# Performance work log

Hardware: AMD Instinct MI355X
Metric: run time of the kernel (lower is better)

The kernel has to match this reference:

```python
import jax, jax.numpy as jnp
import numpy as np

N = 10000
E = 640000


def setup_inputs() -> dict:
    key = jax.random.key(0)
    k = jax.random.split(key, 6)
    x = jax.random.normal(k[0], (N, 128), dtype=jnp.float32)
    edge_index = jax.random.randint(k[1], (2, E), 0, N, dtype=jnp.int64)
    # Linear weights stored as [in, out] (torch stores [out, in]; math is x @ W.T + b)
    w1 = jax.random.normal(k[2], (128, 128), dtype=jnp.float32) * 0.05
    b1 = jax.random.normal(k[3], (128,), dtype=jnp.float32) * 0.05
    w2 = jax.random.normal(k[4], (128, 128), dtype=jnp.float32) * 0.05
    b2 = jax.random.normal(k[5], (128,), dtype=jnp.float32) * 0.05
    return {"x": x, "edge_index": edge_index, "w1": w1, "b1": b1, "w2": w2, "b2": b2}


def gin_conv(x, src, dst, w, b, eps=0.0):
    # aggregate: out[i] = sum over edges (src->dst=i) of x[src]
    agg = jax.ops.segment_sum(x[src], dst, num_segments=N)  # [N, d]
    h = (1.0 + eps) * x + agg
    return h @ w + b


def reference(x, edge_index, w1, b1, w2, b2):
    src, dst = edge_index[0], edge_index[1]
    h = gin_conv(x, src, dst, w1, b1)
    h = jax.nn.relu(h)
    h = gin_conv(h, src, dst, w2, b2)
    return jax.nn.log_softmax(h, axis=1)
```

## Files before the change

kernel.cpp:

```cpp
#include <hip/hip_runtime.h>
#include <cstdint>

#define NNODES 10000
#define FDIM 128
#define MAXDEG 192
#define SLOTS 48

typedef _Float16 h2v  __attribute__((ext_vector_type(2)));
typedef _Float16 f16x8 __attribute__((ext_vector_type(8)));
typedef float    f32x4 __attribute__((ext_vector_type(4)));

__device__ __align__(16)  int      g_cnt[NNODES * 4];
__device__                int      g_bucket[NNODES * MAXDEG];
__device__ __align__(256) unsigned g_xh [(NNODES + 1) * FDIM / 2];
__device__ __align__(256) unsigned g_h1h[(NNODES + 1) * FDIM / 2];
__device__ __align__(16)  unsigned g_wf[2 * 8192];

__device__ inline h2v as_h2(unsigned u) { return __builtin_bit_cast(h2v, u); }
__device__ inline unsigned as_u(h2v v) { return __builtin_bit_cast(unsigned, v); }
__device__ inline unsigned pack_f16x2(float a, float b) {
  h2v v; v[0] = (_Float16)a; v[1] = (_Float16)b;
  return as_u(v);
}
__device__ inline void vadd4(uint4& a, const uint4& b) {
  a.x = as_u(as_h2(a.x) + as_h2(b.x));
  a.y = as_u(as_h2(a.y) + as_h2(b.y));
  a.z = as_u(as_h2(a.z) + as_h2(b.z));
  a.w = as_u(as_h2(a.w) + as_h2(b.w));
}

__global__ __launch_bounds__(256) void prep_kernel(
    const float* __restrict__ x, const int* __restrict__ ei,
    const float* __restrict__ w1, const float* __restrict__ w2,
    int E_, int EBLK, int CBLK) {
  const int bid = blockIdx.x;
  if (bid < EBLK) {
    int e = bid * 256 + threadIdx.x;
    if (e < E_) {
      int d = ei[E_ + e];
      int s = ei[e];
      int st = e & 3;
      int p = atomicAdd(&g_cnt[d * 4 + st], 1);
      if (p < SLOTS) g_bucket[d * MAXDEG + st * SLOTS + p] = s;
    }
  } else if (bid < EBLK + CBLK) {
    int i = (bid - EBLK) * 256 + threadIdx.x;
    if (i < NNODES * FDIM / 2) {
      float2 v = *(const float2*)(x + 2 * (size_t)i);
      g_xh[i] = pack_f16x2(v.x, v.y);
    }
  } else {
    int idx = (bid - EBLK - CBLK) * 256 + threadIdx.x;
    const float* w = (idx >= 2048) ? w2 : w1;
    int s = idx & 2047;
    int sl = s & 63, nk = s >> 6;
    int n = nk >> 2, kc = nk & 3;
    int kbase = kc * 32 + (sl >> 4) * 8;
    int f = n * 16 + (sl & 15);
    unsigned d0 = pack_f16x2(w[(size_t)(kbase + 0) * FDIM + f],
                             w[(size_t)(kbase + 1) * FDIM + f]);
    unsigned d1 = pack_f16x2(w[(size_t)(kbase + 2) * FDIM + f],
                             w[(size_t)(kbase + 3) * FDIM + f]);
    unsigned d2 = pack_f16x2(w[(size_t)(kbase + 4) * FDIM + f],
                             w[(size_t)(kbase + 5) * FDIM + f]);
    unsigned d3 = pack_f16x2(w[(size_t)(kbase + 6) * FDIM + f],
                             w[(size_t)(kbase + 7) * FDIM + f]);
    *(uint4*)(g_wf + (idx >> 11) * 8192 + 4 * s) = make_uint4(d0, d1, d2, d3);
  }
}

template <int MODE>
__global__ __launch_bounds__(512) void gin_layer_kernel(
    const float* __restrict__ b,
    float* __restrict__ out_g) {
  const unsigned* __restrict__ xh = (MODE == 0) ? g_xh : g_h1h;

  __shared__ __align__(16) unsigned wl[8192];
  __shared__ __align__(16) unsigned al[16 * 68];

  const int tid = threadIdx.x;
  const int wave = tid >> 6, lane = tid & 63;
  const int quad = lane >> 4, m16 = lane & 15;
  const int node0 = blockIdx.x * 16;

  {
    const uint4* wf4 = (const uint4*)(g_wf + (MODE ? 8192 : 0));
    uint4* wl4 = (uint4*)wl;
#pragma unroll
    for (int it = 0; it < 4; ++it) wl4[tid + it * 512] = wf4[tid + it * 512];
  }

  const int myn0 = node0 + wave * 2;
  uint4 self4[2];
  int o1[2], o2[2], o3[2], dgg[2];
#pragma unroll
  for (int i = 0; i < 2; ++i) {
    self4[i] = *(const uint4*)(xh + (size_t)(myn0 + i) * 64 + (m16 << 2));
    int4 c = *(const int4*)(g_cnt + (myn0 + i) * 4);
    int a = (c.x > SLOTS) ? SLOTS : c.x;
    int bq = (c.y > SLOTS) ? SLOTS : c.y;
    int cq = (c.z > SLOTS) ? SLOTS : c.z;
    int dq = (c.w > SLOTS) ? SLOTS : c.w;
    o1[i] = a; o2[i] = a + bq; o3[i] = a + bq + cq; dgg[i] = a + bq + cq + dq;
  }

  for (int i = 0; i < 2; ++i) {
    h2v a0 = as_h2(0u), a1 = as_h2(0u), a2 = as_h2(0u), a3 = as_h2(0u);
    const int deg = dgg[i];
    const int* nb = g_bucket + (size_t)(myn0 + i) * MAXDEG;
    for (int p = 0; p < deg; p += 64) {
      int n = deg - p; if (n > 64) n = 64;
      int myedge = NNODES;
      if (lane < n) {
        int g = p + lane;
        int base = 0;
        if (g >= o1[i]) base = o1[i];
        if (g >= o2[i]) base = o2[i];
        if (g >= o3[i]) base = o3[i];
        int st = (g >= o1[i]) + (g >= o2[i]) + (g >= o3[i]);
        myedge = nb[st * SLOTS + (g - base)];
      }
      const int nst = (n + 3) >> 2;
      int s = 0;
      for (; s + 8 <= nst; s += 8) {
        uint4 t[8];
#pragma unroll
        for (int k = 0; k < 8; ++k) {
          int e = __builtin_amdgcn_ds_bpermute((((s + k) << 2) | quad) << 2, myedge);
          t[k] = *(const uint4*)(xh + (unsigned)((e << 6) | (m16 << 2)));
        }
#pragma unroll
        for (int st2 = 1; st2 < 8; st2 <<= 1)
#pragma unroll
          for (int k = 0; k < 8; k += 2 * st2) vadd4(t[k], t[k + st2]);
        a0 += as_h2(t[0].x); a1 += as_h2(t[0].y);
        a2 += as_h2(t[0].z); a3 += as_h2(t[0].w);
      }
      if (s + 4 <= nst) {
        uint4 t[4];
#pragma unroll
        for (int k = 0; k < 4; ++k) {
          int e = __builtin_amdgcn_ds_bpermute((((s + k) << 2) | quad) << 2, myedge);
          t[k] = *(const uint4*)(xh + (unsigned)((e << 6) | (m16 << 2)));
        }
        vadd4(t[0], t[1]); vadd4(t[2], t[3]); vadd4(t[0], t[2]);
        a0 += as_h2(t[0].x); a1 += as_h2(t[0].y);
        a2 += as_h2(t[0].z); a3 += as_h2(t[0].w);
        s += 4;
      }
      for (; s < nst; ++s) {
        int e = __builtin_amdgcn_ds_bpermute(((s << 2) | quad) << 2, myedge);
        uint4 t = *(const uint4*)(xh + (unsigned)((e << 6) | (m16 << 2)));
        a0 += as_h2(t.x); a1 += as_h2(t.y); a2 += as_h2(t.z); a3 += as_h2(t.w);
      }
    }
    int r;
    r = __shfl_xor((int)as_u(a0), 16, 64); a0 += as_h2((unsigned)r);
    r = __shfl_xor((int)as_u(a0), 32, 64); a0 += as_h2((unsigned)r);
    r = __shfl_xor((int)as_u(a1), 16, 64); a1 += as_h2((unsigned)r);
    r = __shfl_xor((int)as_u(a1), 32, 64); a1 += as_h2((unsigned)r);
    r = __shfl_xor((int)as_u(a2), 16, 64); a2 += as_h2((unsigned)r);
    r = __shfl_xor((int)as_u(a2), 32, 64); a2 += as_h2((unsigned)r);
    r = __shfl_xor((int)as_u(a3), 16, 64); a3 += as_h2((unsigned)r);
    r = __shfl_xor((int)as_u(a3), 32, 64); a3 += as_h2((unsigned)r);
    a0 += as_h2(self4[i].x); a1 += as_h2(self4[i].y);
    a2 += as_h2(self4[i].z); a3 += as_h2(self4[i].w);
    if (quad == 0)
      *(uint4*)(al + (wave * 2 + i) * 68 + (m16 << 2)) =
          make_uint4(as_u(a0), as_u(a1), as_u(a2), as_u(a3));
  }
  __syncthreads();

  uint4 af[4];
#pragma unroll
  for (int kc = 0; kc < 4; ++kc)
    af[kc] = *(const uint4*)(al + m16 * 68 + kc * 16 + quad * 4);

  const int n = wave;
  const float bb = b[n * 16 + m16];
  f32x4 acc = {0.f, 0.f, 0.f, 0.f};
#pragma unroll
  for (int kc = 0; kc < 4; ++kc) {
    uint4 bf = *(const uint4*)(wl + ((n * 4 + kc) * 64 + lane) * 4);
    acc = __builtin_amdgcn_mfma_f32_16x16x32_f16(
            __builtin_bit_cast(f16x8, af[kc]),
            __builtin_bit_cast(f16x8, bf), acc, 0, 0, 0);
  }
  __syncthreads();

  if (MODE == 0) {
    _Float16* ch = (_Float16*)wl;
    const int f = n * 16 + m16;
#pragma unroll
    for (int reg = 0; reg < 4; ++reg)
      ch[(quad * 4 + reg) * 136 + f] = (_Float16)fmaxf(acc[reg] + bb, 0.f);
    __syncthreads();
    const int row = tid >> 5, c2 = (tid & 31) * 2;
    uint2 v = *(const uint2*)(wl + row * 68 + c2);
    *(uint2*)(&g_h1h[(size_t)(node0 + row) * 64 + c2]) = v;
  } else {
    float* cf = (float*)wl;
    const int f = n * 16 + m16;
#pragma unroll
    for (int reg = 0; reg < 4; ++reg)
      cf[(quad * 4 + reg) * 132 + f] = acc[reg] + bb;
    __syncthreads();
    const int row = tid >> 5, li = tid & 31;
    const float* base = cf + row * 132 + li * 4;
    float4 a4 = *(const float4*)(base);
    float mx = fmaxf(fmaxf(a4.x, a4.y), fmaxf(a4.z, a4.w));
#pragma unroll
    for (int off = 16; off >= 1; off >>= 1)
      mx = fmaxf(mx, __shfl_xor(mx, off, 64));
    float s = (__expf(a4.x - mx) + __expf(a4.y - mx))
            + (__expf(a4.z - mx) + __expf(a4.w - mx));
#pragma unroll
    for (int off = 16; off >= 1; off >>= 1)
      s += __shfl_xor(s, off, 64);
    const float ls = mx + __logf(s);
    float* orow = out_g + (size_t)(node0 + row) * FDIM + li * 4;
    *(float4*)(orow) = make_float4(a4.x - ls, a4.y - ls, a4.z - ls, a4.w - ls);
    if (tid < 64) g_cnt[node0 * 4 + tid] = 0;
  }
}

extern "C" void kernel_launch(void* const* d_in, const int* in_sizes, int n_in,
                              void* d_out, int out_size, void* d_ws, size_t ws_size,
                              hipStream_t stream) {
  const float* x  = (const float*)d_in[0];
  const int*   ei = (const int*)d_in[1];
  const float* w1 = (const float*)d_in[2];
  const float* b1 = (const float*)d_in[3];
  const float* w2 = (const float*)d_in[4];
  const float* b2 = (const float*)d_in[5];
  float* out = (float*)d_out;

  const int E_ = in_sizes[1] / 2;
  const int EBLK = (E_ + 255) / 256;
  const int CBLK = (NNODES * FDIM / 2 + 255) / 256;
  const int WBLK = 16;

  prep_kernel<<<EBLK + CBLK + WBLK, 256, 0, stream>>>(x, ei, w1, w2, E_, EBLK, CBLK);

  gin_layer_kernel<0><<<625, 512, 0, stream>>>(b1, nullptr);
  gin_layer_kernel<1><<<625, 512, 0, stream>>>(b2, out);
}
```

Before: 126.0 us.

## Fuse prep and both GIN layers into one cooperative persistent kernel

Replaces the three separate launches (prep, layer 0, layer 1) with a single cooperative kernel that uses grid-wide syncs between phases and grid-stride loops over node groups. Weight fragments are now held in registers per wave instead of being staged through shared memory each block, and the x-to-fp16 conversion is vectorised to float4. This removes launch gaps and per-block weight copies, but adds grid barrier cost and caps parallelism at the co-resident block count.

```diff
diff --git a/kernel.cpp b/kernel.cpp
--- a/kernel.cpp
+++ b/kernel.cpp
@@ -1,5 +1,8 @@
 #include <hip/hip_runtime.h>
+#include <hip/hip_cooperative_groups.h>
 #include <cstdint>
+
+namespace cg = cooperative_groups;
 
 #define NNODES 10000
 #define FDIM 128
@@ -29,28 +32,185 @@
   a.w = as_u(as_h2(a.w) + as_h2(b.w));
 }
 
-__global__ __launch_bounds__(256) void prep_kernel(
+template <int MODE>
+__device__ __forceinline__ void layer_phase(
+    const float* __restrict__ bvec, float* __restrict__ out_g,
+    unsigned* __restrict__ al,
+    unsigned* __restrict__ cfu) {
+  const unsigned* __restrict__ xh = (MODE == 0) ? g_xh : g_h1h;
+
+  const int tid = threadIdx.x;
+  const int wave = tid >> 6, lane = tid & 63;
+  const int quad = lane >> 4, m16 = lane & 15;
+
+  uint4 bf[4];
+  {
+    const unsigned* wfp = g_wf + (MODE ? 8192 : 0);
+#pragma unroll
+    for (int kc = 0; kc < 4; ++kc)
+      bf[kc] = *(const uint4*)(wfp + ((wave * 4 + kc) * 64 + lane) * 4);
+  }
+  const float bb = bvec[wave * 16 + m16];
+
+  for (int grp = blockIdx.x; grp < 625; grp += gridDim.x) {
+    const int node0 = grp * 16;
+    const int myn0 = node0 + wave * 2;
+
+    uint4 self4[2];
+    int o1[2], o2[2], o3[2], dgg[2];
+#pragma unroll
+    for (int i = 0; i < 2; ++i) {
+      self4[i] = *(const uint4*)(xh + (size_t)(myn0 + i) * 64 + (m16 << 2));
+      int4 c = *(const int4*)(g_cnt + (myn0 + i) * 4);
+      int a = (c.x > SLOTS) ? SLOTS : c.x;
+      int bq = (c.y > SLOTS) ? SLOTS : c.y;
+      int cq = (c.z > SLOTS) ? SLOTS : c.z;
+      int dq = (c.w > SLOTS) ? SLOTS : c.w;
+      o1[i] = a; o2[i] = a + bq; o3[i] = a + bq + cq; dgg[i] = a + bq + cq + dq;
+    }
+
+    for (int i = 0; i < 2; ++i) {
+      h2v a0 = as_h2(0u), a1 = as_h2(0u), a2 = as_h2(0u), a3 = as_h2(0u);
+      const int deg = dgg[i];
+      const int* nb = g_bucket + (size_t)(myn0 + i) * MAXDEG;
+      for (int p = 0; p < deg; p += 64) {
+        int n = deg - p; if (n > 64) n = 64;
+        int myedge = NNODES;
+        if (lane < n) {
+          int g = p + lane;
+          int base = 0;
+          if (g >= o1[i]) base = o1[i];
+          if (g >= o2[i]) base = o2[i];
+          if (g >= o3[i]) base = o3[i];
+          int st = (g >= o1[i]) + (g >= o2[i]) + (g >= o3[i]);
+          myedge = nb[st * SLOTS + (g - base)];
+        }
+        const int nst = (n + 3) >> 2;
+        int s = 0;
+        for (; s + 8 <= nst; s += 8) {
+          uint4 t[8];
+#pragma unroll
+          for (int k = 0; k < 8; ++k) {
+            int e = __builtin_amdgcn_ds_bpermute((((s + k) << 2) | quad) << 2, myedge);
+            t[k] = *(const uint4*)(xh + (unsigned)((e << 6) | (m16 << 2)));
+          }
+#pragma unroll
+          for (int st2 = 1; st2 < 8; st2 <<= 1)
+#pragma unroll
+            for (int k = 0; k < 8; k += 2 * st2) vadd4(t[k], t[k + st2]);
+          a0 += as_h2(t[0].x); a1 += as_h2(t[0].y);
+          a2 += as_h2(t[0].z); a3 += as_h2(t[0].w);
+        }
+        if (s + 4 <= nst) {
+          uint4 t[4];
+#pragma unroll
+          for (int k = 0; k < 4; ++k) {
+            int e = __builtin_amdgcn_ds_bpermute((((s + k) << 2) | quad) << 2, myedge);
+            t[k] = *(const uint4*)(xh + (unsigned)((e << 6) | (m16 << 2)));
+          }
+          vadd4(t[0], t[1]); vadd4(t[2], t[3]); vadd4(t[0], t[2]);
+          a0 += as_h2(t[0].x); a1 += as_h2(t[0].y);
+          a2 += as_h2(t[0].z); a3 += as_h2(t[0].w);
+          s += 4;
+        }
+        for (; s < nst; ++s) {
+          int e = __builtin_amdgcn_ds_bpermute(((s << 2) | quad) << 2, myedge);
+          uint4 t = *(const uint4*)(xh + (unsigned)((e << 6) | (m16 << 2)));
+          a0 += as_h2(t.x); a1 += as_h2(t.y); a2 += as_h2(t.z); a3 += as_h2(t.w);
+        }
+      }
+      int r;
+      r = __shfl_xor((int)as_u(a0), 16, 64); a0 += as_h2((unsigned)r);
+      r = __shfl_xor((int)as_u(a0), 32, 64); a0 += as_h2((unsigned)r);
+      r = __shfl_xor((int)as_u(a1), 16, 64); a1 += as_h2((unsigned)r);
+      r = __shfl_xor((int)as_u(a1), 32, 64); a1 += as_h2((unsigned)r);
+      r = __shfl_xor((int)as_u(a2), 16, 64); a2 += as_h2((unsigned)r);
+      r = __shfl_xor((int)as_u(a2), 32, 64); a2 += as_h2((unsigned)r);
+      r = __shfl_xor((int)as_u(a3), 16, 64); a3 += as_h2((unsigned)r);
+      r = __shfl_xor((int)as_u(a3), 32, 64); a3 += as_h2((unsigned)r);
+      a0 += as_h2(self4[i].x); a1 += as_h2(self4[i].y);
+      a2 += as_h2(self4[i].z); a3 += as_h2(self4[i].w);
+      if (quad == 0)
+        *(uint4*)(al + (wave * 2 + i) * 68 + (m16 << 2)) =
+            make_uint4(as_u(a0), as_u(a1), as_u(a2), as_u(a3));
+    }
+    __syncthreads();
+
+    uint4 af[4];
+#pragma unroll
+    for (int kc = 0; kc < 4; ++kc)
+      af[kc] = *(const uint4*)(al + m16 * 68 + kc * 16 + quad * 4);
+
+    const int n = wave;
+    f32x4 acc = {0.f, 0.f, 0.f, 0.f};
+#pragma unroll
+    for (int kc = 0; kc < 4; ++kc)
+      acc = __builtin_amdgcn_mfma_f32_16x16x32_f16(
+              __builtin_bit_cast(f16x8, af[kc]),
+              __builtin_bit_cast(f16x8, bf[kc]), acc, 0, 0, 0);
+
+    if (MODE == 0) {
+      _Float16* ch = (_Float16*)cfu;
+      const int f = n * 16 + m16;
+#pragma unroll
+      for (int reg = 0; reg < 4; ++reg)
+        ch[(quad * 4 + reg) * 136 + f] = (_Float16)fmaxf(acc[reg] + bb, 0.f);
+      __syncthreads();
+      const int row = tid >> 5, c2 = (tid & 31) * 2;
+      uint2 v = *(const uint2*)(cfu + row * 68 + c2);
+      *(uint2*)(&g_h1h[(size_t)(node0 + row) * 64 + c2]) = v;
+    } else {
+      float* cf = (float*)cfu;
+      const int f = n * 16 + m16;
+#pragma unroll
+      for (int reg = 0; reg < 4; ++reg)
+        cf[(quad * 4 + reg) * 132 + f] = acc[reg] + bb;
+      __syncthreads();
+      const int row = tid >> 5, li = tid & 31;
+      const float* base = cf + row * 132 + li * 4;
+      float4 a4 = *(const float4*)(base);
+      float mx = fmaxf(fmaxf(a4.x, a4.y), fmaxf(a4.z, a4.w));
+#pragma unroll
+      for (int off = 16; off >= 1; off >>= 1)
+        mx = fmaxf(mx, __shfl_xor(mx, off, 64));
+      float s = (__expf(a4.x - mx) + __expf(a4.y - mx))
+              + (__expf(a4.z - mx) + __expf(a4.w - mx));
+#pragma unroll
+      for (int off = 16; off >= 1; off >>= 1)
+        s += __shfl_xor(s, off, 64);
+      const float ls = mx + __logf(s);
+      float* orow = out_g + (size_t)(node0 + row) * FDIM + li * 4;
+      *(float4*)(orow) = make_float4(a4.x - ls, a4.y - ls, a4.z - ls, a4.w - ls);
+      if (tid < 64) g_cnt[node0 * 4 + tid] = 0;
+    }
+  }
+}
+
+__global__ __launch_bounds__(512, 4) void fused_gin_kernel(
     const float* __restrict__ x, const int* __restrict__ ei,
-    const float* __restrict__ w1, const float* __restrict__ w2,
-    int E_, int EBLK, int CBLK) {
-  const int bid = blockIdx.x;
-  if (bid < EBLK) {
-    int e = bid * 256 + threadIdx.x;
-    if (e < E_) {
-      int d = ei[E_ + e];
-      int s = ei[e];
-      int st = e & 3;
-      int p = atomicAdd(&g_cnt[d * 4 + st], 1);
-      if (p < SLOTS) g_bucket[d * MAXDEG + st * SLOTS + p] = s;
-    }
-  } else if (bid < EBLK + CBLK) {
-    int i = (bid - EBLK) * 256 + threadIdx.x;
-    if (i < NNODES * FDIM / 2) {
-      float2 v = *(const float2*)(x + 2 * (size_t)i);
-      g_xh[i] = pack_f16x2(v.x, v.y);
-    }
-  } else {
-    int idx = (bid - EBLK - CBLK) * 256 + threadIdx.x;
+    const float* __restrict__ w1, const float* __restrict__ b1,
+    const float* __restrict__ w2, const float* __restrict__ b2,
+    float* __restrict__ out, int E_) {
+  __shared__ __align__(16) unsigned s_al[16 * 68];
+  __shared__ __align__(16) unsigned s_cf[16 * 132];
+
+  const int tid = threadIdx.x;
+  const int gsz = gridDim.x * 512;
+  const int gtid = blockIdx.x * 512 + tid;
+
+  for (int e = gtid; e < E_; e += gsz) {
+    int d = ei[E_ + e];
+    int s = ei[e];
+    int st = e & 3;
+    int p = atomicAdd(&g_cnt[d * 4 + st], 1);
+    if (p < SLOTS) g_bucket[d * MAXDEG + st * SLOTS + p] = s;
+  }
+  for (int i = gtid; i < NNODES * 32; i += gsz) {
+    float4 v = *(const float4*)(x + 4 * (size_t)i);
+    uint2 o; o.x = pack_f16x2(v.x, v.y); o.y = pack_f16x2(v.z, v.w);
+    *(uint2*)(g_xh + 2 * (size_t)i) = o;
+  }
+  for (int idx = gtid; idx < 4096; idx += gsz) {
     const float* w = (idx >= 2048) ? w2 : w1;
     int s = idx & 2047;
     int sl = s & 63, nk = s >> 6;
@@ -67,161 +227,11 @@
                              w[(size_t)(kbase + 7) * FDIM + f]);
     *(uint4*)(g_wf + (idx >> 11) * 8192 + 4 * s) = make_uint4(d0, d1, d2, d3);
   }
-}
-
-template <int MODE>
-__global__ __launch_bounds__(512) void gin_layer_kernel(
-    const float* __restrict__ b,
-    float* __restrict__ out_g) {
-  const unsigned* __restrict__ xh = (MODE == 0) ? g_xh : g_h1h;
-
-  __shared__ __align__(16) unsigned wl[8192];
-  __shared__ __align__(16) unsigned al[16 * 68];
-
-  const int tid = threadIdx.x;
-  const int wave = tid >> 6, lane = tid & 63;
-  const int quad = lane >> 4, m16 = lane & 15;
-  const int node0 = blockIdx.x * 16;
-
-  {
-    const uint4* wf4 = (const uint4*)(g_wf + (MODE ? 8192 : 0));
-    uint4* wl4 = (uint4*)wl;
-#pragma unroll
-    for (int it = 0; it < 4; ++it) wl4[tid + it * 512] = wf4[tid + it * 512];
-  }
-
-  const int myn0 = node0 + wave * 2;
-  uint4 self4[2];
-  int o1[2], o2[2], o3[2], dgg[2];
-#pragma unroll
-  for (int i = 0; i < 2; ++i) {
-    self4[i] = *(const uint4*)(xh + (size_t)(myn0 + i) * 64 + (m16 << 2));
-    int4 c = *(const int4*)(g_cnt + (myn0 + i) * 4);
-    int a = (c.x > SLOTS) ? SLOTS : c.x;
-    int bq = (c.y > SLOTS) ? SLOTS : c.y;
-    int cq = (c.z > SLOTS) ? SLOTS : c.z;
-    int dq = (c.w > SLOTS) ? SLOTS : c.w;
-    o1[i] = a; o2[i] = a + bq; o3[i] = a + bq + cq; dgg[i] = a + bq + cq + dq;
-  }
-
-  for (int i = 0; i < 2; ++i) {
-    h2v a0 = as_h2(0u), a1 = as_h2(0u), a2 = as_h2(0u), a3 = as_h2(0u);
-    const int deg = dgg[i];
-    const int* nb = g_bucket + (size_t)(myn0 + i) * MAXDEG;
-    for (int p = 0; p < deg; p += 64) {
-      int n = deg - p; if (n > 64) n = 64;
-      int myedge = NNODES;
-      if (lane < n) {
-        int g = p + lane;
-        int base = 0;
-        if (g >= o1[i]) base = o1[i];
-        if (g >= o2[i]) base = o2[i];
-        if (g >= o3[i]) base = o3[i];
-        int st = (g >= o1[i]) + (g >= o2[i]) + (g >= o3[i]);
-        myedge = nb[st * SLOTS + (g - base)];
-      }
-      const int nst = (n + 3) >> 2;
-      int s = 0;
-      for (; s + 8 <= nst; s += 8) {
-        uint4 t[8];
-#pragma unroll
-        for (int k = 0; k < 8; ++k) {
-          int e = __builtin_amdgcn_ds_bpermute((((s + k) << 2) | quad) << 2, myedge);
-          t[k] = *(const uint4*)(xh + (unsigned)((e << 6) | (m16 << 2)));
-        }
-#pragma unroll
-        for (int st2 = 1; st2 < 8; st2 <<= 1)
-#pragma unroll
-          for (int k = 0; k < 8; k += 2 * st2) vadd4(t[k], t[k + st2]);
-        a0 += as_h2(t[0].x); a1 += as_h2(t[0].y);
-        a2 += as_h2(t[0].z); a3 += as_h2(t[0].w);
-      }
-      if (s + 4 <= nst) {
-        uint4 t[4];
-#pragma unroll
-        for (int k = 0; k < 4; ++k) {
-          int e = __builtin_amdgcn_ds_bpermute((((s + k) << 2) | quad) << 2, myedge);
-          t[k] = *(const uint4*)(xh + (unsigned)((e << 6) | (m16 << 2)));
-        }
-        vadd4(t[0], t[1]); vadd4(t[2], t[3]); vadd4(t[0], t[2]);
-        a0 += as_h2(t[0].x); a1 += as_h2(t[0].y);
-        a2 += as_h2(t[0].z); a3 += as_h2(t[0].w);
-        s += 4;
-      }
-      for (; s < nst; ++s) {
-        int e = __builtin_amdgcn_ds_bpermute(((s << 2) | quad) << 2, myedge);
-        uint4 t = *(const uint4*)(xh + (unsigned)((e << 6) | (m16 << 2)));
-        a0 += as_h2(t.x); a1 += as_h2(t.y); a2 += as_h2(t.z); a3 += as_h2(t.w);
-      }
-    }
-    int r;
-    r = __shfl_xor((int)as_u(a0), 16, 64); a0 += as_h2((unsigned)r);
-    r = __shfl_xor((int)as_u(a0), 32, 64); a0 += as_h2((unsigned)r);
-    r = __shfl_xor((int)as_u(a1), 16, 64); a1 += as_h2((unsigned)r);
-    r = __shfl_xor((int)as_u(a1), 32, 64); a1 += as_h2((unsigned)r);
-    r = __shfl_xor((int)as_u(a2), 16, 64); a2 += as_h2((unsigned)r);
-    r = __shfl_xor((int)as_u(a2), 32, 64); a2 += as_h2((unsigned)r);
-    r = __shfl_xor((int)as_u(a3), 16, 64); a3 += as_h2((unsigned)r);
-    r = __shfl_xor((int)as_u(a3), 32, 64); a3 += as_h2((unsigned)r);
-    a0 += as_h2(self4[i].x); a1 += as_h2(self4[i].y);
-    a2 += as_h2(self4[i].z); a3 += as_h2(self4[i].w);
-    if (quad == 0)
-      *(uint4*)(al + (wave * 2 + i) * 68 + (m16 << 2)) =
-          make_uint4(as_u(a0), as_u(a1), as_u(a2), as_u(a3));
-  }
-  __syncthreads();
-
-  uint4 af[4];
-#pragma unroll
-  for (int kc = 0; kc < 4; ++kc)
-    af[kc] = *(const uint4*)(al + m16 * 68 + kc * 16 + quad * 4);
-
-  const int n = wave;
-  const float bb = b[n * 16 + m16];
-  f32x4 acc = {0.f, 0.f, 0.f, 0.f};
-#pragma unroll
-  for (int kc = 0; kc < 4; ++kc) {
-    uint4 bf = *(const uint4*)(wl + ((n * 4 + kc) * 64 + lane) * 4);
-    acc = __builtin_amdgcn_mfma_f32_16x16x32_f16(
-            __builtin_bit_cast(f16x8, af[kc]),
-            __builtin_bit_cast(f16x8, bf), acc, 0, 0, 0);
-  }
-  __syncthreads();
-
-  if (MODE == 0) {
-    _Float16* ch = (_Float16*)wl;
-    const int f = n * 16 + m16;
-#pragma unroll
-    for (int reg = 0; reg < 4; ++reg)
-      ch[(quad * 4 + reg) * 136 + f] = (_Float16)fmaxf(acc[reg] + bb, 0.f);
-    __syncthreads();
-    const int row = tid >> 5, c2 = (tid & 31) * 2;
-    uint2 v = *(const uint2*)(wl + row * 68 + c2);
-    *(uint2*)(&g_h1h[(size_t)(node0 + row) * 64 + c2]) = v;
-  } else {
-    float* cf = (float*)wl;
-    const int f = n * 16 + m16;
-#pragma unroll
-    for (int reg = 0; reg < 4; ++reg)
-      cf[(quad * 4 + reg) * 132 + f] = acc[reg] + bb;
-    __syncthreads();
-    const int row = tid >> 5, li = tid & 31;
-    const float* base = cf + row * 132 + li * 4;
-    float4 a4 = *(const float4*)(base);
-    float mx = fmaxf(fmaxf(a4.x, a4.y), fmaxf(a4.z, a4.w));
-#pragma unroll
-    for (int off = 16; off >= 1; off >>= 1)
-      mx = fmaxf(mx, __shfl_xor(mx, off, 64));
-    float s = (__expf(a4.x - mx) + __expf(a4.y - mx))
-            + (__expf(a4.z - mx) + __expf(a4.w - mx));
-#pragma unroll
-    for (int off = 16; off >= 1; off >>= 1)
-      s += __shfl_xor(s, off, 64);
-    const float ls = mx + __logf(s);
-    float* orow = out_g + (size_t)(node0 + row) * FDIM + li * 4;
-    *(float4*)(orow) = make_float4(a4.x - ls, a4.y - ls, a4.z - ls, a4.w - ls);
-    if (tid < 64) g_cnt[node0 * 4 + tid] = 0;
-  }
+
+  cg::this_grid().sync();
+  layer_phase<0>(b1, nullptr, s_al, s_cf);
+  cg::this_grid().sync();
+  layer_phase<1>(b2, out, s_al, s_cf);
 }
 
 extern "C" void kernel_launch(void* const* d_in, const int* in_sizes, int n_in,
@@ -234,14 +244,21 @@
   const float* w2 = (const float*)d_in[4];
   const float* b2 = (const float*)d_in[5];
   float* out = (float*)d_out;
-
-  const int E_ = in_sizes[1] / 2;
-  const int EBLK = (E_ + 255) / 256;
-  const int CBLK = (NNODES * FDIM / 2 + 255) / 256;
-  const int WBLK = 16;
-
-  prep_kernel<<<EBLK + CBLK + WBLK, 256, 0, stream>>>(x, ei, w1, w2, E_, EBLK, CBLK);
-
-  gin_layer_kernel<0><<<625, 512, 0, stream>>>(b1, nullptr);
-  gin_layer_kernel<1><<<625, 512, 0, stream>>>(b2, out);
-}
+  int E_ = in_sizes[1] / 2;
+
+  static int nblk = 0;
+  if (nblk == 0) {
+    int per = 0;
+    if (hipOccupancyMaxActiveBlocksPerMultiprocessor(&per, fused_gin_kernel,
+                                                     512, 0) != hipSuccess ||
+        per < 1)
+      per = 1;
+    long cap = (long)per * 256;
+    nblk = (int)(cap < 625 ? cap : 625);
+  }
+
+  void* args[] = {(void*)&x, (void*)&ei, (void*)&w1, (void*)&b1,
+                  (void*)&w2, (void*)&b2, (void*)&out, (void*)&E_};
+  hipLaunchCooperativeKernel((const void*)fused_gin_kernel, dim3(nblk),
+                             dim3(512), args, 0, stream);
+}
```

Measured after the change: 228.9 us. 81.7% more time.
